# Kernel optimization log

Hardware: AMD Instinct MI355X
Metric: run time of the kernel (lower is better)

The kernel has to match this reference:

```python
import jax, jax.numpy as jnp
import numpy as np

N_NODES = 100000
K_HOPS = 10
ALPHA = 0.1


def gcn_conv(x, src, dst, W, b, num_nodes):
    # GCNConv: linear first (cheaper: out_dim small), then D^-1/2 (A+I) D^-1/2 aggregation
    h = x @ W  # [N, out]
    deg = jax.ops.segment_sum(jnp.ones_like(dst, dtype=h.dtype), dst, num_segments=num_nodes)
    dinv = jnp.where(deg > 0, jax.lax.rsqrt(deg), 0.0)
    norm = dinv[src] * dinv[dst]  # [E]
    msg = h[src] * norm[:, None]
    out = jax.ops.segment_sum(msg, dst, num_segments=num_nodes)
    return out + b


def _with_self_loops(edge_index, num_nodes):
    loops = jnp.arange(num_nodes, dtype=edge_index.dtype)
    src = jnp.concatenate([edge_index[0], loops])
    dst = jnp.concatenate([edge_index[1], loops])
    return src, dst


def setup_inputs() -> dict:
    key = jax.random.key(0)
    ks = jax.random.split(key, 8)
    n_feat, hidden, n_cls, n_edges = 512, 16, 7, 3200000
    x = jax.random.normal(ks[0], (N_NODES, n_feat), dtype=jnp.float32)
    edge_index = jax.random.randint(ks[1], (2, n_edges), 0, N_NODES, dtype=jnp.int64)
    W1 = jax.random.normal(ks[2], (n_feat, hidden), dtype=jnp.float32) * 0.05
    b1 = jnp.zeros((hidden,), dtype=jnp.float32)
    Wl = jax.random.normal(ks[3], (hidden, hidden), dtype=jnp.float32) * 0.25
    bl = jnp.zeros((hidden,), dtype=jnp.float32)
    W2 = jax.random.normal(ks[4], (hidden, n_cls), dtype=jnp.float32) * 0.25
    b2 = jnp.zeros((n_cls,), dtype=jnp.float32)
    return {"x": x, "edge_index": edge_index, "W1": W1, "b1": b1, "Wl": Wl, "bl": bl, "W2": W2, "b2": b2}


def reference(x, edge_index, W1, b1, Wl, bl, W2, b2):
    src, dst = _with_self_loops(edge_index, N_NODES)
    h = jax.nn.relu(gcn_conv(x, src, dst, W1, b1, N_NODES))
    def body(h, _):
        h = ALPHA * jax.nn.relu(h @ Wl + bl) + (1.0 - ALPHA) * h
        return h, None
    h, _ = jax.lax.scan(body, h, None, length=K_HOPS)
    out = gcn_conv(h, src, dst, W2, b2, N_NODES)
    return jax.nn.log_softmax(out, axis=1)
```

## Files before the change

### kernel.cpp

```cpp
#include <hip/hip_runtime.h>
#include <math.h>

#define N_NODES 100000
#define N_EDGES 3200000
#define F_IN    512
#define HID     16
#define NCLS    7
#define ALPHA   0.1f
#define K_HOPS  10

#define SHIFT   7
#define BWIDTH  128
#define NBUCK   ((N_NODES + BWIDTH - 1) / BWIDTH)
#define CHUNK   8192
#define EPT     (CHUNK / 256)
#define A3_BLOCKS ((N_EDGES + CHUNK - 1) / CHUNK)

#define OFF_BCNT    0u
#define OFF_BSTART  1024u
#define OFF_BCUR    2048u
#define OFF_RP      3072u
#define OFF_DINV    103424u
#define OFF_COL     203776u
#define OFF_BINNED  3403776u
#define OFF_H0      6603776u
#define OFF_H1      8203776u
#define OFF_Z       9803776u

__global__ void k_bhist(const int* __restrict__ dst, int* __restrict__ bcnt) {
    __shared__ int h[NBUCK];
    int tid = threadIdx.x;
    for (int i = tid; i < NBUCK; i += 256) h[i] = 0;
    __syncthreads();
    for (int e = blockIdx.x * 256 + tid; e < N_EDGES; e += gridDim.x * 256)
        atomicAdd(&h[dst[e] >> SHIFT], 1);
    __syncthreads();
    for (int i = tid; i < NBUCK; i += 256) {
        int v = h[i];
        if (v) atomicAdd(&bcnt[i], v);
    }
}

__global__ void k_bscan(const int* __restrict__ bcnt, int* __restrict__ bstart,
                        int* __restrict__ bcur) {
    __shared__ int s[1024];
    int tid = threadIdx.x;
    int v = (tid < NBUCK) ? bcnt[tid] : 0;
    s[tid] = v;
    __syncthreads();
    for (int off = 1; off < 1024; off <<= 1) {
        int t = (tid >= off) ? s[tid - off] : 0;
        __syncthreads();
        s[tid] += t;
        __syncthreads();
    }
    if (tid < NBUCK) {
        int ex = s[tid] - v;
        bstart[tid] = ex;
        bcur[tid] = ex;
    }
    if (tid == 0) bstart[NBUCK] = N_EDGES;
}

__global__ void k_bin(const int* __restrict__ src, const int* __restrict__ dst,
                      int* __restrict__ bcur, unsigned int* __restrict__ binned) {
    __shared__ int ha[NBUCK];
    __shared__ int gbase[NBUCK];
    __shared__ int lcur[NBUCK];
    int tid = threadIdx.x;
    int e0 = blockIdx.x * CHUNK;
    int e1 = e0 + CHUNK;
    if (e1 > N_EDGES) e1 = N_EDGES;
    for (int i = tid; i < NBUCK; i += 256) ha[i] = 0;
    __syncthreads();
    int dloc[EPT];
#pragma unroll
    for (int i = 0; i < EPT; i++) {
        int e = e0 + tid + i * 256;
        dloc[i] = (e < e1) ? dst[e] : -1;
        if (dloc[i] >= 0) atomicAdd(&ha[dloc[i] >> SHIFT], 1);
    }
    __syncthreads();
    for (int s = tid; s < NBUCK; s += 256) {
        int c = ha[s];
        lcur[s] = 0;
        gbase[s] = c ? atomicAdd(&bcur[s], c) : 0;
    }
    __syncthreads();
#pragma unroll
    for (int i = 0; i < EPT; i++) {
        int d = dloc[i];
        if (d >= 0) {
            int e = e0 + tid + i * 256;
            int bk = d >> SHIFT;
            int idx = atomicAdd(&lcur[bk], 1);
            binned[gbase[bk] + idx] =
                ((unsigned int)(d & (BWIDTH - 1)) << 17) | (unsigned int)src[e];
        }
    }
}

__global__ void k_csr(const unsigned int* __restrict__ binned, const int* __restrict__ bstart,
                      int* __restrict__ rp, float* __restrict__ dinv, int* __restrict__ col) {
    __shared__ int cnt[BWIDTH];
    __shared__ int s[BWIDTH];
    __shared__ int cur[BWIDTH];
    int tid = threadIdx.x;
    int b = blockIdx.x;
    int base = b << SHIFT;
    int e0 = bstart[b], e1 = bstart[b + 1];
    if (tid < BWIDTH) cnt[tid] = 0;
    __syncthreads();
    for (int e = e0 + tid; e < e1; e += 256)
        atomicAdd(&cnt[binned[e] >> 17], 1);
    __syncthreads();
    int v = 0;
    if (tid < BWIDTH) { v = cnt[tid]; s[tid] = v; }
    __syncthreads();
    for (int off = 1; off < BWIDTH; off <<= 1) {
        int t = 0;
        if (tid < BWIDTH && tid >= off) t = s[tid - off];
        __syncthreads();
        if (tid < BWIDTH) s[tid] += t;
        __syncthreads();
    }
    if (tid < BWIDTH) {
        int ex = s[tid] - v;
        cur[tid] = ex;
        int node = base + tid;
        if (node < N_NODES) {
            rp[node] = e0 + ex;
            dinv[node] = rsqrtf((float)(v + 1));
        }
    }
    if (b == 0 && tid == 0) rp[N_NODES] = N_EDGES;
    __syncthreads();
    for (int e = e0 + tid; e < e1; e += 256) {
        unsigned int w = binned[e];
        int ln = (int)(w >> 17);
        int p = atomicAdd(&cur[ln], 1);
        col[e0 + p] = (int)(w & 0x1FFFFu);
    }
}

#define XW_ROWS 64
#define XW_KT   32
#define XW_S    36
#define XW_NT   (F_IN / XW_KT)
__global__ void k_xw1(const float* __restrict__ x, const float* __restrict__ W,
                      const float* __restrict__ dinv, float* __restrict__ h0s) {
    __shared__ float xT[2][XW_ROWS * XW_S];
    int tid = threadIdx.x;
    int rowBase = blockIdx.x * XW_ROWS;

    int rf0 = tid >> 3, kq = tid & 7;
    int rf1 = rf0 + 32;
    bool v0 = (rowBase + rf0) < N_NODES;
    bool v1 = (rowBase + rf1) < N_NODES;
    const float4* xrow0 = (const float4*)(x + (size_t)(rowBase + rf0) * F_IN);
    const float4* xrow1 = (const float4*)(x + (size_t)(rowBase + rf1) * F_IN);

    int r  = tid & 63;
    int cg = __builtin_amdgcn_readfirstlane(tid >> 6);
    const float4* W4 = (const float4*)W;

    float4 zero4 = make_float4(0.f, 0.f, 0.f, 0.f);
    float4 acc = zero4;
    float4 ld0 = v0 ? xrow0[kq] : zero4;
    float4 ld1 = v1 ? xrow1[kq] : zero4;

    for (int kt = 0; kt < XW_NT; kt++) {
        float* xb = xT[kt & 1];
        *(float4*)&xb[rf0 * XW_S + kq * 4] = ld0;
        *(float4*)&xb[rf1 * XW_S + kq * 4] = ld1;
        if (kt + 1 < XW_NT) {
            ld0 = v0 ? xrow0[(kt + 1) * 8 + kq] : zero4;
            ld1 = v1 ? xrow1[(kt + 1) * 8 + kq] : zero4;
        }
        __syncthreads();
        const float* xr = &xb[r * XW_S];
#pragma unroll
        for (int k8 = 0; k8 < 8; k8++) {
            float4 xv = *(const float4*)&xr[k8 * 4];
            float4 w0 = W4[(kt * XW_KT + k8 * 4 + 0) * 4 + cg];
            acc.x += xv.x * w0.x; acc.y += xv.x * w0.y;
            acc.z += xv.x * w0.z; acc.w += xv.x * w0.w;
            float4 w1 = W4[(kt * XW_KT + k8 * 4 + 1) * 4 + cg];
            acc.x += xv.y * w1.x; acc.y += xv.y * w1.y;
            acc.z += xv.y * w1.z; acc.w += xv.y * w1.w;
            float4 w2 = W4[(kt * XW_KT + k8 * 4 + 2) * 4 + cg];
            acc.x += xv.z * w2.x; acc.y += xv.z * w2.y;
            acc.z += xv.z * w2.z; acc.w += xv.z * w2.w;
            float4 w3 = W4[(kt * XW_KT + k8 * 4 + 3) * 4 + cg];
            acc.x += xv.w * w3.x; acc.y += xv.w * w3.y;
            acc.z += xv.w * w3.z; acc.w += xv.w * w3.w;
        }
        __syncthreads();
    }
    int node = rowBase + r;
    if (node < N_NODES) {
        float dv = dinv[node];
        float4 o;
        o.x = dv * acc.x; o.y = dv * acc.y; o.z = dv * acc.z; o.w = dv * acc.w;
        ((float4*)h0s)[(size_t)node * 4 + cg] = o;
    }
}

__global__ void k_agg1(const float* __restrict__ h0s, const int* __restrict__ rp,
                       const int* __restrict__ col, const float* __restrict__ dinv,
                       const float* __restrict__ b1, float* __restrict__ h1) {
    int node = (blockIdx.x * blockDim.x + threadIdx.x) >> 6;
    if (node >= N_NODES) return;
    int lane = threadIdx.x & 63;
    int c = lane & 15, eo = lane >> 4;
    int e0 = rp[node], e1 = rp[node + 1];
    float acc = 0.f;
    int e = e0 + eo;
    for (; e + 4 < e1; e += 8) {
        int c0 = col[e];
        int c1 = col[e + 4];
        float v0 = h0s[(size_t)c0 * HID + c];
        float v1 = h0s[(size_t)c1 * HID + c];
        acc += v0;
        acc += v1;
    }
    if (e < e1) acc += h0s[(size_t)col[e] * HID + c];
    acc += __shfl_xor(acc, 16);
    acc += __shfl_xor(acc, 32);
    float o = dinv[node] * (acc + h0s[(size_t)node * HID + c]) + b1[c];
    if (eo == 0) h1[(size_t)node * HID + c] = fmaxf(o, 0.f);
}

__global__ void k_hops(const float* __restrict__ h1, const float* __restrict__ Wl,
                       const float* __restrict__ bl, const float* __restrict__ W2,
                       const float* __restrict__ dinv, float* __restrict__ zs) {
    int node = blockIdx.x * blockDim.x + threadIdx.x;
    if (node >= N_NODES) return;
    float h[HID];
    const float4* h4 = (const float4*)(h1 + (size_t)node * HID);
#pragma unroll
    for (int q = 0; q < HID / 4; q++) {
        float4 v = h4[q];
        h[q * 4 + 0] = v.x; h[q * 4 + 1] = v.y;
        h[q * 4 + 2] = v.z; h[q * 4 + 3] = v.w;
    }
    for (int it = 0; it < K_HOPS; it++) {
        float tm[HID];
#pragma unroll
        for (int c = 0; c < HID; c++) tm[c] = bl[c];
#pragma unroll
        for (int k = 0; k < HID; k++) {
            float hk = h[k];
#pragma unroll
            for (int c = 0; c < HID; c++) tm[c] += hk * Wl[k * HID + c];
        }
#pragma unroll
        for (int c = 0; c < HID; c++)
            h[c] = ALPHA * fmaxf(tm[c], 0.f) + (1.f - ALPHA) * h[c];
    }
    float dv = dinv[node];
    float zz[8];
#pragma unroll
    for (int c = 0; c < 8; c++) zz[c] = 0.f;
#pragma unroll
    for (int k = 0; k < HID; k++) {
        float hk = h[k];
#pragma unroll
        for (int c = 0; c < NCLS; c++) zz[c] += hk * W2[k * NCLS + c];
    }
    float4* z4 = (float4*)(zs + (size_t)node * 8);
    float4 v0, v1;
    v0.x = dv * zz[0]; v0.y = dv * zz[1]; v0.z = dv * zz[2]; v0.w = dv * zz[3];
    v1.x = dv * zz[4]; v1.y = dv * zz[5]; v1.z = dv * zz[6]; v1.w = 0.f;
    z4[0] = v0; z4[1] = v1;
}

__global__ void k_agg2(const float* __restrict__ zs, const int* __restrict__ rp,
                       const int* __restrict__ col, const float* __restrict__ dinv,
                       const float* __restrict__ b2, float* __restrict__ out) {
    int node = (blockIdx.x * blockDim.x + threadIdx.x) >> 6;
    if (node >= N_NODES) return;
    int lane = threadIdx.x & 63;
    int c = lane & 7, eo = lane >> 3;
    int e0 = rp[node], e1 = rp[node + 1];
    float acc = 0.f;
    int e = e0 + eo;
    for (; e + 8 < e1; e += 16) {
        int c0 = col[e];
        int c1 = col[e + 8];
        float v0 = zs[(size_t)c0 * 8 + c];
        float v1 = zs[(size_t)c1 * 8 + c];
        acc += v0;
        acc += v1;
    }
    if (e < e1) acc += zs[(size_t)col[e] * 8 + c];
    acc += __shfl_xor(acc, 8);
    acc += __shfl_xor(acc, 16);
    acc += __shfl_xor(acc, 32);
    float o = dinv[node] * (acc + zs[(size_t)node * 8 + c]) + ((c < NCLS) ? b2[c] : 0.f);
    float val = (c < NCLS) ? o : -INFINITY;
    float m = val;
    m = fmaxf(m, __shfl_xor(m, 1));
    m = fmaxf(m, __shfl_xor(m, 2));
    m = fmaxf(m, __shfl_xor(m, 4));
    float ex = (c < NCLS) ? expf(o - m) : 0.f;
    float ss = ex;
    ss += __shfl_xor(ss, 1);
    ss += __shfl_xor(ss, 2);
    ss += __shfl_xor(ss, 4);
    if (eo == 0 && c < NCLS) out[(size_t)node * NCLS + c] = o - m - logf(ss);
}

extern "C" void kernel_launch(void* const* d_in, const int* in_sizes, int n_in,
                              void* d_out, int out_size, void* d_ws, size_t ws_size,
                              hipStream_t stream) {
    const float* x  = (const float*)d_in[0];
    const int*   ei = (const int*)d_in[1];
    const float* W1 = (const float*)d_in[2];
    const float* b1 = (const float*)d_in[3];
    const float* Wl = (const float*)d_in[4];
    const float* bl = (const float*)d_in[5];
    const float* W2 = (const float*)d_in[6];
    const float* b2 = (const float*)d_in[7];
    float* out = (float*)d_out;

    int*   wsI = (int*)d_ws;
    float* wsF = (float*)d_ws;
    int*          bcnt   = wsI + OFF_BCNT;
    int*          bstart = wsI + OFF_BSTART;
    int*          bcur   = wsI + OFF_BCUR;
    int*          rp     = wsI + OFF_RP;
    float*        dinv   = wsF + OFF_DINV;
    int*          col    = wsI + OFF_COL;
    unsigned int* binned = (unsigned int*)(wsI + OFF_BINNED);
    float*        h0s    = wsF + OFF_H0;
    float*        h1     = wsF + OFF_H1;
    float*        zs     = wsF + OFF_Z;

    const int* src = ei;
    const int* dst = ei + N_EDGES;

    hipMemsetAsync(bcnt, 0, NBUCK * sizeof(int), stream);

    k_bhist<<<1024, 256, 0, stream>>>(dst, bcnt);
    k_bscan<<<1, 1024, 0, stream>>>(bcnt, bstart, bcur);
    k_bin<<<A3_BLOCKS, 256, 0, stream>>>(src, dst, bcur, binned);
    k_csr<<<NBUCK, 256, 0, stream>>>(binned, bstart, rp, dinv, col);
    k_xw1<<<(N_NODES + XW_ROWS - 1) / XW_ROWS, 256, 0, stream>>>(x, W1, dinv, h0s);
    k_agg1<<<(N_NODES * 64 + 255) / 256, 256, 0, stream>>>(h0s, rp, col, dinv, b1, h1);
    k_hops<<<(N_NODES + 255) / 256, 256, 0, stream>>>(h1, Wl, bl, W2, dinv, zs);
    k_agg2<<<(N_NODES * 64 + 255) / 256, 256, 0, stream>>>(zs, rp, col, dinv, b2, out);
}
```

Baseline: 578.2 us.

## Build CSR via global-atomic degree count and scatter instead of bucketed binning

Replaces the two-level bucket binning CSR construction (bucket histogram, bucket scan, binning, per-bucket local sort) with a direct approach: global atomic degree histogram, two-pass block scan, and an atomic scatter of source ids into col. This drops the intermediate binned buffer and one full pass over the edges. In exchange it relies on 3.2M scattered global atomics, which could contend and produces a nondeterministic ordering of neighbours within each row, and it loses the locality of the bucketed writes.

After: 831.9 us. +43.9%, slower.

```diff
diff --git a/kernel.cpp b/kernel.cpp
--- a/kernel.cpp
+++ b/kernel.cpp
@@ -9,138 +9,75 @@
 #define ALPHA   0.1f
 #define K_HOPS  10
 
-#define SHIFT   7
-#define BWIDTH  128
-#define NBUCK   ((N_NODES + BWIDTH - 1) / BWIDTH)
-#define CHUNK   8192
-#define EPT     (CHUNK / 256)
-#define A3_BLOCKS ((N_EDGES + CHUNK - 1) / CHUNK)
-
-#define OFF_BCNT    0u
-#define OFF_BSTART  1024u
-#define OFF_BCUR    2048u
-#define OFF_RP      3072u
-#define OFF_DINV    103424u
-#define OFF_COL     203776u
-#define OFF_BINNED  3403776u
-#define OFF_H0      6603776u
-#define OFF_H1      8203776u
-#define OFF_Z       9803776u
-
-__global__ void k_bhist(const int* __restrict__ dst, int* __restrict__ bcnt) {
-    __shared__ int h[NBUCK];
+#define OFF_DEG     0u
+#define OFF_PART    100352u
+#define OFF_CUR     101376u
+#define OFF_RP      202752u
+#define OFF_DINV    303104u
+#define OFF_COL     403456u
+#define OFF_H0      3603456u
+#define OFF_H1      5203456u
+#define OFF_Z       6803456u
+
+#define SCB 1024
+#define SCG ((N_NODES + SCB - 1) / SCB)
+
+__global__ void k_deg(const int* __restrict__ dst, int* __restrict__ deg) {
+    int t = blockIdx.x * 256 + threadIdx.x;
+    const int4* d4 = (const int4*)dst;
+    int4 d = d4[t];
+    atomicAdd(&deg[d.x], 1);
+    atomicAdd(&deg[d.y], 1);
+    atomicAdd(&deg[d.z], 1);
+    atomicAdd(&deg[d.w], 1);
+}
+
+__global__ void k_scan1(const int* __restrict__ deg, int* __restrict__ rp,
+                        int* __restrict__ part) {
+    __shared__ int s[SCB];
     int tid = threadIdx.x;
-    for (int i = tid; i < NBUCK; i += 256) h[i] = 0;
-    __syncthreads();
-    for (int e = blockIdx.x * 256 + tid; e < N_EDGES; e += gridDim.x * 256)
-        atomicAdd(&h[dst[e] >> SHIFT], 1);
-    __syncthreads();
-    for (int i = tid; i < NBUCK; i += 256) {
-        int v = h[i];
-        if (v) atomicAdd(&bcnt[i], v);
-    }
-}
-
-__global__ void k_bscan(const int* __restrict__ bcnt, int* __restrict__ bstart,
-                        int* __restrict__ bcur) {
-    __shared__ int s[1024];
-    int tid = threadIdx.x;
-    int v = (tid < NBUCK) ? bcnt[tid] : 0;
+    int i = blockIdx.x * SCB + tid;
+    int v = (i < N_NODES) ? deg[i] : 0;
     s[tid] = v;
     __syncthreads();
-    for (int off = 1; off < 1024; off <<= 1) {
+    for (int off = 1; off < SCB; off <<= 1) {
         int t = (tid >= off) ? s[tid - off] : 0;
         __syncthreads();
         s[tid] += t;
         __syncthreads();
     }
-    if (tid < NBUCK) {
-        int ex = s[tid] - v;
-        bstart[tid] = ex;
-        bcur[tid] = ex;
-    }
-    if (tid == 0) bstart[NBUCK] = N_EDGES;
-}
-
-__global__ void k_bin(const int* __restrict__ src, const int* __restrict__ dst,
-                      int* __restrict__ bcur, unsigned int* __restrict__ binned) {
-    __shared__ int ha[NBUCK];
-    __shared__ int gbase[NBUCK];
-    __shared__ int lcur[NBUCK];
-    int tid = threadIdx.x;
-    int e0 = blockIdx.x * CHUNK;
-    int e1 = e0 + CHUNK;
-    if (e1 > N_EDGES) e1 = N_EDGES;
-    for (int i = tid; i < NBUCK; i += 256) ha[i] = 0;
-    __syncthreads();
-    int dloc[EPT];
-#pragma unroll
-    for (int i = 0; i < EPT; i++) {
-        int e = e0 + tid + i * 256;
-        dloc[i] = (e < e1) ? dst[e] : -1;
-        if (dloc[i] >= 0) atomicAdd(&ha[dloc[i] >> SHIFT], 1);
-    }
-    __syncthreads();
-    for (int s = tid; s < NBUCK; s += 256) {
-        int c = ha[s];
-        lcur[s] = 0;
-        gbase[s] = c ? atomicAdd(&bcur[s], c) : 0;
-    }
-    __syncthreads();
-#pragma unroll
-    for (int i = 0; i < EPT; i++) {
-        int d = dloc[i];
-        if (d >= 0) {
-            int e = e0 + tid + i * 256;
-            int bk = d >> SHIFT;
-            int idx = atomicAdd(&lcur[bk], 1);
-            binned[gbase[bk] + idx] =
-                ((unsigned int)(d & (BWIDTH - 1)) << 17) | (unsigned int)src[e];
-        }
-    }
-}
-
-__global__ void k_csr(const unsigned int* __restrict__ binned, const int* __restrict__ bstart,
-                      int* __restrict__ rp, float* __restrict__ dinv, int* __restrict__ col) {
-    __shared__ int cnt[BWIDTH];
-    __shared__ int s[BWIDTH];
-    __shared__ int cur[BWIDTH];
-    int tid = threadIdx.x;
-    int b = blockIdx.x;
-    int base = b << SHIFT;
-    int e0 = bstart[b], e1 = bstart[b + 1];
-    if (tid < BWIDTH) cnt[tid] = 0;
-    __syncthreads();
-    for (int e = e0 + tid; e < e1; e += 256)
-        atomicAdd(&cnt[binned[e] >> 17], 1);
-    __syncthreads();
-    int v = 0;
-    if (tid < BWIDTH) { v = cnt[tid]; s[tid] = v; }
-    __syncthreads();
-    for (int off = 1; off < BWIDTH; off <<= 1) {
-        int t = 0;
-        if (tid < BWIDTH && tid >= off) t = s[tid - off];
-        __syncthreads();
-        if (tid < BWIDTH) s[tid] += t;
-        __syncthreads();
-    }
-    if (tid < BWIDTH) {
-        int ex = s[tid] - v;
-        cur[tid] = ex;
-        int node = base + tid;
-        if (node < N_NODES) {
-            rp[node] = e0 + ex;
-            dinv[node] = rsqrtf((float)(v + 1));
-        }
-    }
-    if (b == 0 && tid == 0) rp[N_NODES] = N_EDGES;
-    __syncthreads();
-    for (int e = e0 + tid; e < e1; e += 256) {
-        unsigned int w = binned[e];
-        int ln = (int)(w >> 17);
-        int p = atomicAdd(&cur[ln], 1);
-        col[e0 + p] = (int)(w & 0x1FFFFu);
-    }
+    if (i < N_NODES) rp[i] = s[tid] - v;
+    if (tid == SCB - 1) part[blockIdx.x] = s[tid];
+}
+
+__global__ void k_scan2(const int* __restrict__ part, const int* __restrict__ deg,
+                        int* __restrict__ rp, int* __restrict__ cur,
+                        float* __restrict__ dinv) {
+    int b = blockIdx.x, tid = threadIdx.x;
+    int i = b * SCB + tid;
+    int base = 0;
+    for (int j = 0; j < b; j++) base += part[j];
+    if (i < N_NODES) {
+        int r = rp[i] + base;
+        rp[i] = r;
+        cur[i] = r;
+        dinv[i] = rsqrtf((float)(deg[i] + 1));
+    }
+    if (i == N_NODES) rp[N_NODES] = N_EDGES;
+}
+
+__global__ void k_scat(const int* __restrict__ src, const int* __restrict__ dst,
+                       int* __restrict__ cur, int* __restrict__ col) {
+    int t = blockIdx.x * 256 + threadIdx.x;
+    const int4* s4 = (const int4*)src;
+    const int4* d4 = (const int4*)dst;
+    int4 s = s4[t];
+    int4 d = d4[t];
+    int p;
+    p = atomicAdd(&cur[d.x], 1); col[p] = s.x;
+    p = atomicAdd(&cur[d.y], 1); col[p] = s.y;
+    p = atomicAdd(&cur[d.z], 1); col[p] = s.z;
+    p = atomicAdd(&cur[d.w], 1); col[p] = s.w;
 }
 
 #define XW_ROWS 64
@@ -326,26 +263,25 @@
 
     int*   wsI = (int*)d_ws;
     float* wsF = (float*)d_ws;
-    int*          bcnt   = wsI + OFF_BCNT;
-    int*          bstart = wsI + OFF_BSTART;
-    int*          bcur   = wsI + OFF_BCUR;
-    int*          rp     = wsI + OFF_RP;
-    float*        dinv   = wsF + OFF_DINV;
-    int*          col    = wsI + OFF_COL;
-    unsigned int* binned = (unsigned int*)(wsI + OFF_BINNED);
-    float*        h0s    = wsF + OFF_H0;
-    float*        h1     = wsF + OFF_H1;
-    float*        zs     = wsF + OFF_Z;
+    int*   deg  = wsI + OFF_DEG;
+    int*   part = wsI + OFF_PART;
+    int*   cur  = wsI + OFF_CUR;
+    int*   rp   = wsI + OFF_RP;
+    float* dinv = wsF + OFF_DINV;
+    int*   col  = wsI + OFF_COL;
+    float* h0s  = wsF + OFF_H0;
+    float* h1   = wsF + OFF_H1;
+    float* zs   = wsF + OFF_Z;
 
     const int* src = ei;
     const int* dst = ei + N_EDGES;
 
-    hipMemsetAsync(bcnt, 0, NBUCK * sizeof(int), stream);
-
-    k_bhist<<<1024, 256, 0, stream>>>(dst, bcnt);
-    k_bscan<<<1, 1024, 0, stream>>>(bcnt, bstart, bcur);
-    k_bin<<<A3_BLOCKS, 256, 0, stream>>>(src, dst, bcur, binned);
-    k_csr<<<NBUCK, 256, 0, stream>>>(binned, bstart, rp, dinv, col);
+    hipMemsetAsync(deg, 0, N_NODES * sizeof(int), stream);
+
+    k_deg<<<(N_EDGES / 4) / 256, 256, 0, stream>>>(dst, deg);
+    k_scan1<<<SCG, SCB, 0, stream>>>(deg, rp, part);
+    k_scan2<<<SCG, SCB, 0, stream>>>(part, deg, rp, cur, dinv);
+    k_scat<<<(N_EDGES / 4) / 256, 256, 0, stream>>>(src, dst, cur, col);
     k_xw1<<<(N_NODES + XW_ROWS - 1) / XW_ROWS, 256, 0, stream>>>(x, W1, dinv, h0s);
     k_agg1<<<(N_NODES * 64 + 255) / 256, 256, 0, stream>>>(h0s, rp, col, dinv, b1, h1);
     k_hops<<<(N_NODES + 255) / 256, 256, 0, stream>>>(h1, Wl, bl, W2, dinv, zs);
```
